# Performance work log

Hardware: AMD Instinct MI355X
Metric: run time of the kernel (lower is better)

Reference implementation:

```python
import jax, jax.numpy as jnp
import numpy as np

NEG_SLOPE = 0.1

def leaky(x):
    return jnp.where(x >= 0, x, NEG_SLOPE * x)

def setup_inputs() -> dict:
    key = jax.random.key(0)
    ks = jax.random.split(key, 9)
    B, N, K, Cin, Cout = 4, 16384, 16, 64, 128
    xyz = jax.random.normal(ks[0], (B, 3, N), jnp.float32)
    features = jax.random.normal(ks[1], (B, Cin, N), jnp.float32)
    knn_indices = jax.random.randint(ks[2], (B, N, K), 0, N)
    # weight_net: MLP2d(3, [8,16]) == two 1x1 convs with leaky_relu
    w1 = jax.random.normal(ks[3], (8, 3), jnp.float32) * 0.3
    b1 = jax.random.normal(ks[4], (8,), jnp.float32) * 0.05
    w2 = jax.random.normal(ks[5], (16, 8), jnp.float32) * 0.2
    b2 = jax.random.normal(ks[6], (16,), jnp.float32) * 0.05
    lin_w = jax.random.normal(ks[7], (Cout, 16 * (Cin + 3)), jnp.float32) * 0.02
    lin_b = jax.random.normal(ks[8], (Cout,), jnp.float32) * 0.02
    return {"xyz": xyz, "features": features, "knn_indices": knn_indices,
            "w1": w1, "b1": b1, "w2": w2, "b2": b2,
            "lin_w": lin_w, "lin_b": lin_b}

def reference(xyz, features, knn_indices, w1, b1, w2, b2, lin_w, lin_b):
    B, _, N = xyz.shape
    K = knn_indices.shape[2]
    # channel-last views
    xyz_cl = xyz.transpose(0, 2, 1)                                  # [B,N,3]
    feats_cl = jnp.concatenate([xyz, features], axis=1).transpose(0, 2, 1)  # [B,N,3+C]
    gather = jax.vmap(lambda f, i: f[i])                             # per-batch gather
    knn_xyz = gather(xyz_cl, knn_indices)                            # [B,N,K,3]
    knn_xyz_norm = knn_xyz - xyz_cl[:, :, None, :]                   # [B,N,K,3]
    # weight_net (1x1 conv MLP: 3 -> 8 -> 16, leaky_relu)
    h = leaky(jnp.einsum('bnkc,oc->bnko', knn_xyz_norm, w1) + b1)    # [B,N,K,8]
    w = leaky(jnp.einsum('bnkh,oh->bnko', h, w2) + b2)               # [B,N,K,16]
    knn_feats = gather(feats_cl, knn_indices)                        # [B,N,K,3+C]
    # weights^T @ knn_features, flattened (16, 3+C) -> 16*(3+C)
    agg = jnp.einsum('bnkw,bnkc->bnwc', w, knn_feats).reshape(B, N, -1)
    out = leaky(agg @ lin_w.T + lin_b)                               # [B,N,Cout]
    return out.transpose(0, 2, 1)                                    # [B,Cout,N]
```

## Files before the change

### kernel.cpp

```cpp
#include <hip/hip_runtime.h>
#include <hip/hip_bf16.h>

#define B_    4
#define N_    16384
#define K_    16
#define CIN_  64
#define CF_   67
#define COUT_ 128
#define AGGP_ 1088
#define P_    32
#define PH_   16
#define FSTR  72
#define ASTR  1096
#define WTS   272
#define NEG_  0.1f

typedef __attribute__((ext_vector_type(8))) short short8;
typedef __attribute__((ext_vector_type(4))) float f32x4;
typedef __attribute__((ext_vector_type(2))) unsigned int uint2_t;
typedef __attribute__((ext_vector_type(4))) unsigned int uint4_t;

__device__ __forceinline__ unsigned short f2b(float f) {
    __hip_bfloat16 h = __float2bfloat16(f);
    return *reinterpret_cast<unsigned short*>(&h);
}
__device__ __forceinline__ float leaky(float x) { return x >= 0.f ? x : NEG_ * x; }

__global__ __launch_bounds__(256) void pc_prep(
    const float* __restrict__ xyz,
    const float* __restrict__ feats,
    const float* __restrict__ lin_w,
    unsigned short* __restrict__ ft,
    short* __restrict__ lwb)
{
    const int bid = blockIdx.x, t = threadIdx.x;
    if (bid < 1024) {
        __shared__ float st[64][69];
        const int b  = bid >> 8;
        const int j0 = (bid & 255) << 6;
        for (int ii = t; ii < 68 * 16; ii += 256) {
            const int c = ii >> 4, jq = ii & 15;
            f32x4 v = {0.f, 0.f, 0.f, 0.f};
            if (c < 3)
                v = *(const f32x4*)(xyz   + ((size_t)b * 3    + c)       * N_ + j0 + 4 * jq);
            else if (c < CF_)
                v = *(const f32x4*)(feats + ((size_t)b * CIN_ + (c - 3)) * N_ + j0 + 4 * jq);
            st[4 * jq + 0][c] = v.x;
            st[4 * jq + 1][c] = v.y;
            st[4 * jq + 2][c] = v.z;
            st[4 * jq + 3][c] = v.w;
        }
        __syncthreads();
        uint4_t* outp4 = (uint4_t*)(ft + (size_t)(b * N_ + j0) * FSTR);
        for (int idx = t; idx < 64 * 9; idx += 256) {
            const int j2 = idx / 9, q = idx - 9 * j2;
            const int cb = q * 8;
            unsigned u[4];
#pragma unroll
            for (int e = 0; e < 4; e++) {
                const int c0 = cb + 2 * e;
                const unsigned lo = (c0     < CF_) ? (unsigned)f2b(st[j2][c0])     : 0u;
                const unsigned hi = (c0 + 1 < CF_) ? (unsigned)f2b(st[j2][c0 + 1]) : 0u;
                u[e] = lo | (hi << 16);
            }
            uint4_t uu = { u[0], u[1], u[2], u[3] };
            outp4[idx] = uu;
        }
    } else {
        const int o = bid - 1024;
        const float* src = lin_w + (size_t)o * (16 * CF_);
        short*       dst = lwb   + (size_t)o * AGGP_;
        for (int i = t; i < AGGP_; i += 256) {
            const int w = i / 68, c = i % 68;
            dst[i] = (c < CF_) ? (short)f2b(src[w * CF_ + c]) : (short)0;
        }
    }
}

__global__ __launch_bounds__(256, 2) void pc_main(
    const float*          __restrict__ xyz,
    const unsigned short* __restrict__ ft,
    const int*            __restrict__ knn,
    const float* __restrict__ w1, const float* __restrict__ b1,
    const float* __restrict__ w2, const float* __restrict__ b2,
    const short* __restrict__ lwb, const float* __restrict__ lin_b,
    float* __restrict__ out)
{
    __shared__ __align__(16) short s_agg[P_ * ASTR];
    __shared__ __align__(16) short s_WT[PH_ * WTS];
    __shared__ int s_idx[PH_ * K_];

    const int t   = threadIdx.x;
    const int bid = blockIdx.x;
    const int b   = bid >> 9;
    const int n0  = (bid & 511) << 5;
    const unsigned short* ftb = ft + (size_t)b * N_ * FSTR;

#pragma unroll
    for (int h = 0; h < 2; h++) {
        {
            const int p = t >> 4, k = t & 15;
            const int pp = h * PH_ + p;
            const int n = n0 + pp;
            const int j = knn[((size_t)(b * N_ + n)) * K_ + k];
            s_idx[p * K_ + k] = j;
            const float* xb = xyz + (size_t)b * 3 * N_;
            const float dx0 = xb[j]          - xb[n];
            const float dx1 = xb[N_ + j]     - xb[N_ + n];
            const float dx2 = xb[2 * N_ + j] - xb[2 * N_ + n];
            float hh[8];
#pragma unroll
            for (int i = 0; i < 8; i++)
                hh[i] = leaky(b1[i] + w1[i*3+0]*dx0 + w1[i*3+1]*dx1 + w1[i*3+2]*dx2);
            short* wd = s_WT + p * WTS + k;
#pragma unroll
            for (int w = 0; w < 16; w++) {
                float a = b2[w];
#pragma unroll
                for (int i = 0; i < 8; i++) a += w2[w*8+i] * hh[i];
                wd[w * 16] = (short)f2b(leaky(a));
            }
        }
        __asm__ __volatile__("" ::: "memory");

        {
            const int p = t >> 4, s = t & 15;
            const int pp = h * PH_ + p;
            const int* ip = s_idx + p * K_;
            const bool tl = (s < 3);
            uint2_t fb[K_];
            unsigned feu[8] = {0,0,0,0,0,0,0,0};
#pragma unroll
            for (int k = 0; k < K_; k++) {
                const unsigned short* rec = ftb + (size_t)ip[k] * FSTR;
                fb[k] = *(const uint2_t*)(rec + 4 * s);
                if (tl) feu[k >> 1] |= ((unsigned)rec[64 + s]) << (16 * (k & 1));
            }
            short* frow = s_agg + (size_t)pp * ASTR;
            const int hf = ((s >> 2) & 1) << 3;
#pragma unroll
            for (int i = 0; i < 4; i++) {
                const unsigned sel = (i & 1) ? 0x07060302u : 0x05040100u;
                unsigned pk[8];
#pragma unroll
                for (int d = 0; d < 8; d++) {
                    const unsigned lo = (i < 2) ? fb[2*d].x   : fb[2*d].y;
                    const unsigned hi = (i < 2) ? fb[2*d+1].x : fb[2*d+1].y;
                    pk[d] = __builtin_amdgcn_perm(hi, lo, sel);
                }
                const int c   = 4 * s + i;
                const int row = c ^ (s & 3);
                uint4_t q0 = { pk[0], pk[1], pk[2], pk[3] };
                uint4_t q1 = { pk[4], pk[5], pk[6], pk[7] };
                *(uint4_t*)(frow + row * 16 + hf)       = q0;
                *(uint4_t*)(frow + row * 16 + (8 - hf)) = q1;
            }
            if (tl) {
                uint4_t q0 = { feu[0], feu[1], feu[2], feu[3] };
                uint4_t q1 = { feu[4], feu[5], feu[6], feu[7] };
                *(uint4_t*)(frow + (64 + s) * 16)     = q0;
                *(uint4_t*)(frow + (64 + s) * 16 + 8) = q1;
            }
            if (s == 3) {
                uint4_t z = {0u, 0u, 0u, 0u};
                *(uint4_t*)(frow + 67 * 16)     = z;
                *(uint4_t*)(frow + 67 * 16 + 8) = z;
            }
        }
        __asm__ __volatile__("" ::: "memory");

        {
            const int lane = t & 63;
            const int wq   = lane >> 4;
            const int pr   = lane & 15;
            const int pbl  = (t >> 6) * 4;
            const int kh   = (wq & 1) * 8;
            const int side = (wq < 2) ? 0 : 1;
            const int asid = (pr < 8) ? 0 : 1;
            const bool act = (side == asid);
            const int cq   = 4 * (wq & 1);
            const int c0   = pr & 7;
            const int bb   = c0 >> 2;
#pragma unroll
            for (int pair = 0; pair < 2; pair++) {
                const int lpA = pbl + 2 * pair;
                const int ppA = h * PH_ + lpA;
                const short8 bfr = *(const short8*)(s_WT + (lpA + side) * WTS + pr * 16 + kh);
                const short* ap  = s_agg + (size_t)(ppA + asid) * ASTR;
                f32x4 D[9];
#pragma unroll
                for (int cc = 0; cc < 9; cc++) {
                    const int row  = (c0 + 8 * cc) ^ ((bb + 2 * cc) & 3);
                    const int khcc = kh ^ (((cc >> 1) & 1) << 3);
                    short8 af = {0,0,0,0,0,0,0,0};
                    if (act && (cc < 8 || c0 < 4))
                        af = *(const short8*)(ap + row * 16 + khcc);
                    D[cc] = __builtin_amdgcn_mfma_f32_16x16x32_bf16(
                                af, bfr, (f32x4){0.f,0.f,0.f,0.f}, 0, 0, 0);
                }
                __asm__ __volatile__("" ::: "memory");
                short* arow = s_agg + (size_t)(ppA + side) * ASTR + pr * 68;
#pragma unroll
                for (int cc = 0; cc < 9; cc++) {
                    if (cc == 8 && cq != 0) continue;
                    const unsigned lo = (unsigned)f2b(D[cc].x) | ((unsigned)f2b(D[cc].y) << 16);
                    const unsigned hi = (unsigned)f2b(D[cc].z) | ((unsigned)f2b(D[cc].w) << 16);
                    uint2_t pk2 = { lo, hi };
                    *(uint2_t*)(arow + 8 * cc + cq) = pk2;
                }
            }
        }
        __asm__ __volatile__("" ::: "memory");
    }

    {
        const int lane = t & 63, wid = t >> 6;
        const int quad = lane >> 4, pr = lane & 15;
        const int kq = quad * 8;
        const short* a0p = lwb + (size_t)(wid * 32 + pr) * AGGP_ + kq;
        const short* a1p = a0p + 16 * AGGP_;

        short8 pa0[6], pa1[6];
#pragma unroll
        for (int d = 0; d < 6; d++) {
            pa0[d] = *(const short8*)(a0p + 32 * d);
            pa1[d] = *(const short8*)(a1p + 32 * d);
        }
        __syncthreads();

        const short* bp0 = s_agg + (size_t)pr * ASTR + kq;
        const short* bp1 = s_agg + (size_t)(16 + pr) * ASTR + kq;
        f32x4 acc00 = {0.f, 0.f, 0.f, 0.f};
        f32x4 acc01 = {0.f, 0.f, 0.f, 0.f};
        f32x4 acc10 = {0.f, 0.f, 0.f, 0.f};
        f32x4 acc11 = {0.f, 0.f, 0.f, 0.f};

#pragma unroll
        for (int ks = 0; ks < 34; ks++) {
            const int d = ks % 6;
            const short8 a0c = pa0[d], a1c = pa1[d];
            if (ks + 6 < 34) {
                pa0[d] = *(const short8*)(a0p + 32 * (ks + 6));
                pa1[d] = *(const short8*)(a1p + 32 * (ks + 6));
            }
            const short8 b0 = *(const short8*)(bp0 + 32 * ks);
            const short8 b1 = *(const short8*)(bp1 + 32 * ks);
            acc00 = __builtin_amdgcn_mfma_f32_16x16x32_bf16(a0c, b0, acc00, 0, 0, 0);
            acc01 = __builtin_amdgcn_mfma_f32_16x16x32_bf16(a0c, b1, acc01, 0, 0, 0);
            acc10 = __builtin_amdgcn_mfma_f32_16x16x32_bf16(a1c, b0, acc10, 0, 0, 0);
            acc11 = __builtin_amdgcn_mfma_f32_16x16x32_bf16(a1c, b1, acc11, 0, 0, 0);
        }
        const int o0 = wid * 32 + quad * 4;
#pragma unroll
        for (int r = 0; r < 4; r++) {
            const int oA = o0 + r;
            const int oB = oA + 16;
            const float bA = lin_b[oA], bB = lin_b[oB];
            float* rowA = out + ((size_t)(b * COUT_ + oA)) * N_ + n0;
            float* rowB = out + ((size_t)(b * COUT_ + oB)) * N_ + n0;
            rowA[pr]      = leaky(acc00[r] + bA);
            rowA[16 + pr] = leaky(acc01[r] + bA);
            rowB[pr]      = leaky(acc10[r] + bB);
            rowB[16 + pr] = leaky(acc11[r] + bB);
        }
    }
}

extern "C" void kernel_launch(void* const* d_in, const int* in_sizes, int n_in,
                              void* d_out, int out_size, void* d_ws, size_t ws_size,
                              hipStream_t stream)
{
    const float* xyz   = (const float*)d_in[0];
    const float* feats = (const float*)d_in[1];
    const int*   knn   = (const int*)d_in[2];
    const float* w1    = (const float*)d_in[3];
    const float* b1    = (const float*)d_in[4];
    const float* w2    = (const float*)d_in[5];
    const float* b2    = (const float*)d_in[6];
    const float* lin_w = (const float*)d_in[7];
    const float* lin_b = (const float*)d_in[8];
    float* out = (float*)d_out;

    unsigned short* ft = (unsigned short*)d_ws;
    short* lwb = (short*)((char*)d_ws + (size_t)B_ * N_ * FSTR * sizeof(short));

    hipLaunchKernelGGL(pc_prep, dim3(1024 + COUT_), dim3(256), 0, stream,
                       xyz, feats, lin_w, ft, lwb);
    hipLaunchKernelGGL(pc_main, dim3(B_ * (N_ / P_)), dim3(256), 0, stream,
                       xyz, ft, knn, w1, b1, w2, b2, lwb, lin_b, out);
}
```

Before: 220.7 us.

## Issue both halves' feature gathers up front and pack xyz into float4 records

The prep kernel now also writes an xyz array with a 16-byte stride, so each neighbor's coordinates come from one vector load instead of three scattered scalar loads. The main kernel loads the knn indices and coordinate deltas for both 16-point halves at the start, then issues every global feature gather for both halves before the MLP, transpose and MFMA stages run. This aims to hide gather latency behind compute by having more loads in flight at once. The cost is roughly double the gather register footprint (fbA and fbB), which under the 2-waves occupancy bound may cause spills.

```diff
diff --git a/kernel.cpp b/kernel.cpp
--- a/kernel.cpp
+++ b/kernel.cpp
@@ -31,7 +31,8 @@
     const float* __restrict__ feats,
     const float* __restrict__ lin_w,
     unsigned short* __restrict__ ft,
-    short* __restrict__ lwb)
+    short* __restrict__ lwb,
+    float* __restrict__ xyz3)
 {
     const int bid = blockIdx.x, t = threadIdx.x;
     if (bid < 1024) {
@@ -51,6 +52,10 @@
             st[4 * jq + 3][c] = v.w;
         }
         __syncthreads();
+        if (t < 64) {
+            f32x4 v = { st[t][0], st[t][1], st[t][2], 0.f };
+            *(f32x4*)(xyz3 + ((size_t)(b * N_ + j0 + t)) * 4) = v;
+        }
         uint4_t* outp4 = (uint4_t*)(ft + (size_t)(b * N_ + j0) * FSTR);
         for (int idx = t; idx < 64 * 9; idx += 256) {
             const int j2 = idx / 9, q = idx - 9 * j2;
@@ -77,8 +82,114 @@
     }
 }
 
+__device__ __forceinline__ void gather_ft(const unsigned short* ftb, const int* ip,
+                                          int s, bool tl, uint2_t* fb, unsigned* feu)
+{
+#pragma unroll
+    for (int k = 0; k < K_; k++) {
+        const unsigned short* rec = ftb + (size_t)ip[k] * FSTR;
+        fb[k] = *(const uint2_t*)(rec + 4 * s);
+        if (tl) feu[k >> 1] |= ((unsigned)rec[64 + s]) << (16 * (k & 1));
+    }
+}
+
+__device__ __forceinline__ void mlp_store(
+    short* wd, float d0, float d1, float d2,
+    const float* w1, const float* b1, const float* w2, const float* b2)
+{
+    float hh[8];
+#pragma unroll
+    for (int i = 0; i < 8; i++)
+        hh[i] = leaky(b1[i] + w1[i*3+0]*d0 + w1[i*3+1]*d1 + w1[i*3+2]*d2);
+#pragma unroll
+    for (int w = 0; w < 16; w++) {
+        float a = b2[w];
+#pragma unroll
+        for (int i = 0; i < 8; i++) a += w2[w*8+i] * hh[i];
+        wd[w * 16] = (short)f2b(leaky(a));
+    }
+}
+
+__device__ __forceinline__ void transpose_store(
+    short* frow, const uint2_t* fb, const unsigned* feu, int s, bool tl)
+{
+    const int hf = ((s >> 2) & 1) << 3;
+#pragma unroll
+    for (int i = 0; i < 4; i++) {
+        const unsigned sel = (i & 1) ? 0x07060302u : 0x05040100u;
+        unsigned pk[8];
+#pragma unroll
+        for (int d = 0; d < 8; d++) {
+            const unsigned lo = (i < 2) ? fb[2*d].x   : fb[2*d].y;
+            const unsigned hi = (i < 2) ? fb[2*d+1].x : fb[2*d+1].y;
+            pk[d] = __builtin_amdgcn_perm(hi, lo, sel);
+        }
+        const int c   = 4 * s + i;
+        const int row = c ^ (s & 3);
+        uint4_t q0 = { pk[0], pk[1], pk[2], pk[3] };
+        uint4_t q1 = { pk[4], pk[5], pk[6], pk[7] };
+        *(uint4_t*)(frow + row * 16 + hf)       = q0;
+        *(uint4_t*)(frow + row * 16 + (8 - hf)) = q1;
+    }
+    if (tl) {
+        uint4_t q0 = { feu[0], feu[1], feu[2], feu[3] };
+        uint4_t q1 = { feu[4], feu[5], feu[6], feu[7] };
+        *(uint4_t*)(frow + (64 + s) * 16)     = q0;
+        *(uint4_t*)(frow + (64 + s) * 16 + 8) = q1;
+    }
+    if (s == 3) {
+        uint4_t z = {0u, 0u, 0u, 0u};
+        *(uint4_t*)(frow + 67 * 16)     = z;
+        *(uint4_t*)(frow + 67 * 16 + 8) = z;
+    }
+}
+
+__device__ __forceinline__ void agg_mfma(short* s_aggp, const short* s_WTp,
+                                         int t, int pbase)
+{
+    const int lane = t & 63;
+    const int wq   = lane >> 4;
+    const int pr   = lane & 15;
+    const int pbl  = (t >> 6) * 4;
+    const int kh   = (wq & 1) * 8;
+    const int side = (wq < 2) ? 0 : 1;
+    const int asid = (pr < 8) ? 0 : 1;
+    const bool act = (side == asid);
+    const int cq   = 4 * (wq & 1);
+    const int c0   = pr & 7;
+    const int bb   = c0 >> 2;
+#pragma unroll
+    for (int pair = 0; pair < 2; pair++) {
+        const int lpA = pbl + 2 * pair;
+        const int ppA = pbase + lpA;
+        const short8 bfr = *(const short8*)(s_WTp + (lpA + side) * WTS + pr * 16 + kh);
+        const short* ap  = s_aggp + (size_t)(ppA + asid) * ASTR;
+        f32x4 D[9];
+#pragma unroll
+        for (int cc = 0; cc < 9; cc++) {
+            const int row  = (c0 + 8 * cc) ^ ((bb + 2 * cc) & 3);
+            const int khcc = kh ^ (((cc >> 1) & 1) << 3);
+            short8 af = {0,0,0,0,0,0,0,0};
+            if (act && (cc < 8 || c0 < 4))
+                af = *(const short8*)(ap + row * 16 + khcc);
+            D[cc] = __builtin_amdgcn_mfma_f32_16x16x32_bf16(
+                        af, bfr, (f32x4){0.f,0.f,0.f,0.f}, 0, 0, 0);
+        }
+        __asm__ __volatile__("" ::: "memory");
+        short* arow = s_aggp + (size_t)(ppA + side) * ASTR + pr * 68;
+#pragma unroll
+        for (int cc = 0; cc < 9; cc++) {
+            if (cc == 8 && cq != 0) continue;
+            const unsigned lo = (unsigned)f2b(D[cc].x) | ((unsigned)f2b(D[cc].y) << 16);
+            const unsigned hi = (unsigned)f2b(D[cc].z) | ((unsigned)f2b(D[cc].w) << 16);
+            uint2_t pk2 = { lo, hi };
+            *(uint2_t*)(arow + 8 * cc + cq) = pk2;
+        }
+    }
+}
+
 __global__ __launch_bounds__(256, 2) void pc_main(
-    const float*          __restrict__ xyz,
+    const float*          __restrict__ x3,
     const unsigned short* __restrict__ ft,
     const int*            __restrict__ knn,
     const float* __restrict__ w1, const float* __restrict__ b1,
@@ -88,130 +199,49 @@
 {
     __shared__ __align__(16) short s_agg[P_ * ASTR];
     __shared__ __align__(16) short s_WT[PH_ * WTS];
-    __shared__ int s_idx[PH_ * K_];
+    __shared__ int s_idx[2 * PH_ * K_];
 
     const int t   = threadIdx.x;
     const int bid = blockIdx.x;
     const int b   = bid >> 9;
     const int n0  = (bid & 511) << 5;
     const unsigned short* ftb = ft + (size_t)b * N_ * FSTR;
-
-#pragma unroll
-    for (int h = 0; h < 2; h++) {
-        {
-            const int p = t >> 4, k = t & 15;
-            const int pp = h * PH_ + p;
-            const int n = n0 + pp;
-            const int j = knn[((size_t)(b * N_ + n)) * K_ + k];
-            s_idx[p * K_ + k] = j;
-            const float* xb = xyz + (size_t)b * 3 * N_;
-            const float dx0 = xb[j]          - xb[n];
-            const float dx1 = xb[N_ + j]     - xb[N_ + n];
-            const float dx2 = xb[2 * N_ + j] - xb[2 * N_ + n];
-            float hh[8];
-#pragma unroll
-            for (int i = 0; i < 8; i++)
-                hh[i] = leaky(b1[i] + w1[i*3+0]*dx0 + w1[i*3+1]*dx1 + w1[i*3+2]*dx2);
-            short* wd = s_WT + p * WTS + k;
-#pragma unroll
-            for (int w = 0; w < 16; w++) {
-                float a = b2[w];
-#pragma unroll
-                for (int i = 0; i < 8; i++) a += w2[w*8+i] * hh[i];
-                wd[w * 16] = (short)f2b(leaky(a));
-            }
-        }
-        __asm__ __volatile__("" ::: "memory");
-
-        {
-            const int p = t >> 4, s = t & 15;
-            const int pp = h * PH_ + p;
-            const int* ip = s_idx + p * K_;
-            const bool tl = (s < 3);
-            uint2_t fb[K_];
-            unsigned feu[8] = {0,0,0,0,0,0,0,0};
-#pragma unroll
-            for (int k = 0; k < K_; k++) {
-                const unsigned short* rec = ftb + (size_t)ip[k] * FSTR;
-                fb[k] = *(const uint2_t*)(rec + 4 * s);
-                if (tl) feu[k >> 1] |= ((unsigned)rec[64 + s]) << (16 * (k & 1));
-            }
-            short* frow = s_agg + (size_t)pp * ASTR;
-            const int hf = ((s >> 2) & 1) << 3;
-#pragma unroll
-            for (int i = 0; i < 4; i++) {
-                const unsigned sel = (i & 1) ? 0x07060302u : 0x05040100u;
-                unsigned pk[8];
-#pragma unroll
-                for (int d = 0; d < 8; d++) {
-                    const unsigned lo = (i < 2) ? fb[2*d].x   : fb[2*d].y;
-                    const unsigned hi = (i < 2) ? fb[2*d+1].x : fb[2*d+1].y;
-                    pk[d] = __builtin_amdgcn_perm(hi, lo, sel);
-                }
-                const int c   = 4 * s + i;
-                const int row = c ^ (s & 3);
-                uint4_t q0 = { pk[0], pk[1], pk[2], pk[3] };
-                uint4_t q1 = { pk[4], pk[5], pk[6], pk[7] };
-                *(uint4_t*)(frow + row * 16 + hf)       = q0;
-                *(uint4_t*)(frow + row * 16 + (8 - hf)) = q1;
-            }
-            if (tl) {
-                uint4_t q0 = { feu[0], feu[1], feu[2], feu[3] };
-                uint4_t q1 = { feu[4], feu[5], feu[6], feu[7] };
-                *(uint4_t*)(frow + (64 + s) * 16)     = q0;
-                *(uint4_t*)(frow + (64 + s) * 16 + 8) = q1;
-            }
-            if (s == 3) {
-                uint4_t z = {0u, 0u, 0u, 0u};
-                *(uint4_t*)(frow + 67 * 16)     = z;
-                *(uint4_t*)(frow + 67 * 16 + 8) = z;
-            }
-        }
-        __asm__ __volatile__("" ::: "memory");
-
-        {
-            const int lane = t & 63;
-            const int wq   = lane >> 4;
-            const int pr   = lane & 15;
-            const int pbl  = (t >> 6) * 4;
-            const int kh   = (wq & 1) * 8;
-            const int side = (wq < 2) ? 0 : 1;
-            const int asid = (pr < 8) ? 0 : 1;
-            const bool act = (side == asid);
-            const int cq   = 4 * (wq & 1);
-            const int c0   = pr & 7;
-            const int bb   = c0 >> 2;
-#pragma unroll
-            for (int pair = 0; pair < 2; pair++) {
-                const int lpA = pbl + 2 * pair;
-                const int ppA = h * PH_ + lpA;
-                const short8 bfr = *(const short8*)(s_WT + (lpA + side) * WTS + pr * 16 + kh);
-                const short* ap  = s_agg + (size_t)(ppA + asid) * ASTR;
-                f32x4 D[9];
-#pragma unroll
-                for (int cc = 0; cc < 9; cc++) {
-                    const int row  = (c0 + 8 * cc) ^ ((bb + 2 * cc) & 3);
-                    const int khcc = kh ^ (((cc >> 1) & 1) << 3);
-                    short8 af = {0,0,0,0,0,0,0,0};
-                    if (act && (cc < 8 || c0 < 4))
-                        af = *(const short8*)(ap + row * 16 + khcc);
-                    D[cc] = __builtin_amdgcn_mfma_f32_16x16x32_bf16(
-                                af, bfr, (f32x4){0.f,0.f,0.f,0.f}, 0, 0, 0);
-                }
-                __asm__ __volatile__("" ::: "memory");
-                short* arow = s_agg + (size_t)(ppA + side) * ASTR + pr * 68;
-#pragma unroll
-                for (int cc = 0; cc < 9; cc++) {
-                    if (cc == 8 && cq != 0) continue;
-                    const unsigned lo = (unsigned)f2b(D[cc].x) | ((unsigned)f2b(D[cc].y) << 16);
-                    const unsigned hi = (unsigned)f2b(D[cc].z) | ((unsigned)f2b(D[cc].w) << 16);
-                    uint2_t pk2 = { lo, hi };
-                    *(uint2_t*)(arow + 8 * cc + cq) = pk2;
-                }
-            }
-        }
-        __asm__ __volatile__("" ::: "memory");
-    }
+    const f32x4* x3b = (const f32x4*)x3 + (size_t)b * N_;
+
+    const int p = t >> 4, s = t & 15;
+    const bool tl = (s < 3);
+
+    const int n_a = n0 + p, n_b = n0 + PH_ + p;
+    const int ja = knn[((size_t)(b * N_ + n_a)) * K_ + s];
+    const int jb = knn[((size_t)(b * N_ + n_b)) * K_ + s];
+    s_idx[(0 * PH_ + p) * K_ + s] = ja;
+    s_idx[(1 * PH_ + p) * K_ + s] = jb;
+    const f32x4 qa = x3b[ja], qb = x3b[jb];
+    const f32x4 ca = x3b[n_a], cb = x3b[n_b];
+    const float dxa0 = qa.x - ca.x, dxa1 = qa.y - ca.y, dxa2 = qa.z - ca.z;
+    const float dxb0 = qb.x - cb.x, dxb1 = qb.y - cb.y, dxb2 = qb.z - cb.z;
+    __asm__ __volatile__("" ::: "memory");
+
+    const int* ipa = s_idx + (0 * PH_ + p) * K_;
+    const int* ipb = s_idx + (1 * PH_ + p) * K_;
+    uint2_t fbA[K_], fbB[K_];
+    unsigned feuA[8] = {0,0,0,0,0,0,0,0};
+    unsigned feuB[8] = {0,0,0,0,0,0,0,0};
+    gather_ft(ftb, ipa, s, tl, fbA, feuA);
+    gather_ft(ftb, ipb, s, tl, fbB, feuB);
+
+    mlp_store(s_WT + p * WTS + s, dxa0, dxa1, dxa2, w1, b1, w2, b2);
+    __asm__ __volatile__("" ::: "memory");
+    transpose_store(s_agg + (size_t)p * ASTR, fbA, feuA, s, tl);
+    __asm__ __volatile__("" ::: "memory");
+    agg_mfma(s_agg, s_WT, t, 0);
+    __asm__ __volatile__("" ::: "memory");
+
+    mlp_store(s_WT + p * WTS + s, dxb0, dxb1, dxb2, w1, b1, w2, b2);
+    __asm__ __volatile__("" ::: "memory");
+    transpose_store(s_agg + (size_t)(PH_ + p) * ASTR, fbB, feuB, s, tl);
+    __asm__ __volatile__("" ::: "memory");
+    agg_mfma(s_agg, s_WT, t, PH_);
 
     {
         const int lane = t & 63, wid = t >> 6;
@@ -281,11 +311,14 @@
     const float* lin_b = (const float*)d_in[8];
     float* out = (float*)d_out;
 
-    unsigned short* ft = (unsigned short*)d_ws;
-    short* lwb = (short*)((char*)d_ws + (size_t)B_ * N_ * FSTR * sizeof(short));
+    const size_t ftBytes  = (size_t)B_ * N_ * FSTR * sizeof(short);
+    const size_t lwbBytes = (size_t)COUT_ * AGGP_ * sizeof(short);
+    unsigned short* ft   = (unsigned short*)d_ws;
+    short*          lwb  = (short*)((char*)d_ws + ftBytes);
+    float*          xyz3 = (float*)((char*)d_ws + ftBytes + lwbBytes);
 
     hipLaunchKernelGGL(pc_prep, dim3(1024 + COUT_), dim3(256), 0, stream,
-                       xyz, feats, lin_w, ft, lwb);
+                       xyz, feats, lin_w, ft, lwb, xyz3);
     hipLaunchKernelGGL(pc_main, dim3(B_ * (N_ / P_)), dim3(256), 0, stream,
-                       xyz, ft, knn, w1, b1, w2, b2, lwb, lin_b, out);
-}
+                       xyz3, ft, knn, w1, b1, w2, b2, lwb, lin_b, out);
+}
```

Result: faster. 206.8 us (-6.3%).
